# Performance work log

Measured on AMD Instinct MI355X. Metric: run time of the kernel, lower is better.

Reference implementation:

```python
import jax, jax.numpy as jnp
import numpy as np

# NF4 codebook (bitsandbytes nf4 quant_type), 16 levels in [-1, 1]
NF4 = jnp.array([
    -1.0, -0.6961928009986877, -0.5250730514526367, -0.39491748809814453,
    -0.28444138169288635, -0.18477343022823334, -0.09105003625154495, 0.0,
    0.07958029955625534, 0.16093020141124725, 0.24611230194568634,
    0.33791524171829224, 0.44070982933044434, 0.5626170039176941,
    0.7229568362236023, 1.0], dtype=jnp.float32)
BLOCK = 64  # bitsandbytes default quant block size

TOKENS, HD, M = 8192, 4096, 11008


def dequant_nf4(codes, scales):
    # codes: [out, in] int in [0,16); scales: [out, in//BLOCK] per-block absmax
    out_f, in_f = codes.shape
    w = NF4[codes].reshape(out_f, in_f // BLOCK, BLOCK) * scales[:, :, None]
    return w.reshape(out_f, in_f)


def setup_inputs() -> dict:
    key = jax.random.key(0)
    k = jax.random.split(key, 7)
    return {
        "x": jax.random.normal(k[0], (TOKENS, HD), dtype=jnp.float32),
        "gate_codes": jax.random.randint(k[1], (M, HD), 0, 16, dtype=jnp.int32),
        "gate_scales": jax.random.uniform(k[2], (M, HD // BLOCK), dtype=jnp.float32) * 0.1,
        "up_codes": jax.random.randint(k[3], (M, HD), 0, 16, dtype=jnp.int32),
        "up_scales": jax.random.uniform(k[4], (M, HD // BLOCK), dtype=jnp.float32) * 0.1,
        "down_codes": jax.random.randint(k[5], (HD, M), 0, 16, dtype=jnp.int32),
        "down_scales": jax.random.uniform(k[6], (HD, M // BLOCK), dtype=jnp.float32) * 0.1,
    }


def reference(x, gate_codes, gate_scales, up_codes, up_scales, down_codes, down_scales):
    Wg = dequant_nf4(gate_codes, gate_scales)   # [m, hd]
    Wu = dequant_nf4(up_codes, up_scales)       # [m, hd]
    Wd = dequant_nf4(down_codes, down_scales)   # [hd, m]
    g = jnp.einsum('td,md->tm', x, Wg)          # gate_proj(x)
    u = jnp.einsum('td,md->tm', x, Wu)          # up_proj(x)
    h = jax.nn.silu(g) * u                      # SwiGLU
    return jnp.einsum('tm,dm->td', h, Wd)       # down_proj
```

## Files before the change

kernel.cpp:

```cpp
#include <hip/hip_runtime.h>
#include <hip/hip_bf16.h>

typedef _Float16 half8 __attribute__((ext_vector_type(8)));
typedef float floatx4 __attribute__((ext_vector_type(4)));

__device__ __constant__ float NF4_TAB[16] = {
    -1.0f, -0.6961928009986877f, -0.5250730514526367f, -0.39491748809814453f,
    -0.28444138169288635f, -0.18477343022823334f, -0.09105003625154495f, 0.0f,
    0.07958029955625534f, 0.16093020141124725f, 0.24611230194568634f,
    0.33791524171829224f, 0.44070982933044434f, 0.5626170039176941f,
    0.7229568362236023f, 1.0f};

typedef __attribute__((address_space(3))) void lds_t;
typedef __attribute__((address_space(1))) void gbl_t;

__device__ __forceinline__ void gload16(const void* g, void* l) {
  __builtin_amdgcn_global_load_lds((gbl_t*)g, (lds_t*)l, 16, 0, 0);
}

#define FENCE() asm volatile("" ::: "memory")

__global__ void cvt_f32_to_f16_pad(const float* __restrict__ in,
                                   _Float16* __restrict__ out,
                                   int total8, int C8, int OS) {
  int stride = gridDim.x * blockDim.x;
  for (int i = blockIdx.x * blockDim.x + threadIdx.x; i < total8; i += stride) {
    int row = i / C8;
    int col = (i - row * C8) * 8;
    const float4* ip = reinterpret_cast<const float4*>(in + (long)row * (C8 * 8) + col);
    float4 a = ip[0], b = ip[1];
    half8 o;
    o[0] = (_Float16)a.x; o[1] = (_Float16)a.y;
    o[2] = (_Float16)a.z; o[3] = (_Float16)a.w;
    o[4] = (_Float16)b.x; o[5] = (_Float16)b.y;
    o[6] = (_Float16)b.z; o[7] = (_Float16)b.w;
    *reinterpret_cast<half8*>(out + (long)row * OS + col) = o;
  }
}

__global__ void dequant_nf4(const int* __restrict__ codes,
                            const float* __restrict__ scales,
                            _Float16* __restrict__ out,
                            int total8, int C, int CB, int OS) {
  __shared__ float lut[16];
  if (threadIdx.x < 16) lut[threadIdx.x] = NF4_TAB[threadIdx.x];
  __syncthreads();
  int stride = gridDim.x * blockDim.x;
  for (int i = blockIdx.x * blockDim.x + threadIdx.x; i < total8; i += stride) {
    long e = (long)i * 8;
    int row = (int)(e / C);
    int col = (int)(e - (long)row * C);
    float sc = scales[row * CB + (col >> 6)];
    const int4* cp = reinterpret_cast<const int4*>(codes + e);
    int4 c0 = cp[0];
    int4 c1 = cp[1];
    half8 o;
    o[0] = (_Float16)(lut[c0.x & 15] * sc);
    o[1] = (_Float16)(lut[c0.y & 15] * sc);
    o[2] = (_Float16)(lut[c0.z & 15] * sc);
    o[3] = (_Float16)(lut[c0.w & 15] * sc);
    o[4] = (_Float16)(lut[c1.x & 15] * sc);
    o[5] = (_Float16)(lut[c1.y & 15] * sc);
    o[6] = (_Float16)(lut[c1.z & 15] * sc);
    o[7] = (_Float16)(lut[c1.w & 15] * sc);
    *reinterpret_cast<half8*>(out + (long)row * OS + col) = o;
  }
}

template <int K, int LD, int N>
__global__ __launch_bounds__(512, 2) void gemm_fused(
    const _Float16* __restrict__ A,
    const _Float16* __restrict__ G,
    const _Float16* __restrict__ U,
    _Float16* __restrict__ GH) {
  constexpr int NT = K / 64;
  __shared__ __align__(16) _Float16 lds[2 * 32768];

  const int t = threadIdx.x;
  const int lane = t & 63;
  const int wave = t >> 6;
  const int wm = wave >> 2;
  const int wn = wave & 3;

  const int xcd = blockIdx.x & 7;
  const int j = blockIdx.x >> 3;
  const int bm = 4 * xcd + (j & 3);
  const int bn = j >> 2;

  const int lc = (t & 3) ^ ((t >> 3) & 3);
  const _Float16* gA = A + ((long)bm * 256 + (t >> 2)) * LD + lc * 8;
  const _Float16* gG = G + ((long)bn * 128 + (t >> 2)) * LD + lc * 8;
  const _Float16* gU = U + ((long)bn * 128 + (t >> 2)) * LD + lc * 8;
  const long rstep = (long)128 * LD;
  const int dst = t * 8;

  const int rA = wm * 128 + (lane & 15);
  const int rB = wn * 32 + (lane & 15);
  const int ckA = ((lane >> 4) ^ ((rA >> 1) & 3)) * 8;
  const int ckB = ((lane >> 4) ^ ((rB >> 1) & 3)) * 8;
  const int offA = rA * 32 + ckA;
  const int offBG = 16384 + rB * 32 + ckB;
  const int offBU = 24576 + rB * 32 + ckB;

  gload16(gA, lds + dst);
  gload16(gA + rstep, lds + dst + 4096);
  gload16(gG, lds + 16384 + dst);
  gload16(gU, lds + 24576 + dst);
  gload16(gA + 32, lds + 8192 + dst);
  gload16(gA + 32 + rstep, lds + 8192 + dst + 4096);
  gload16(gG + 32, lds + 20480 + dst);
  gload16(gU + 32, lds + 28672 + dst);
  gA += 64; gG += 64; gU += 64;
  asm volatile("s_waitcnt vmcnt(4)" ::: "memory");
  __builtin_amdgcn_s_barrier();
  FENCE();

  floatx4 accG[8][2] = {};
  floatx4 accU[8][2] = {};

  for (int kt = 0; kt < NT; ++kt) {
    const int cb = kt & 1;
    const int sbuf = cb ^ 1;
    const _Float16* lb = lds + cb * 32768;
    _Float16* sb = lds + sbuf * 32768;
    const bool st = (kt + 1 < NT);
    const bool last = (kt == NT - 1);

    half8 a[8], b[2];

#pragma unroll
    for (int i = 0; i < 8; ++i)
      a[i] = *reinterpret_cast<const half8*>(&lb[offA + i * 512]);
    b[0] = *reinterpret_cast<const half8*>(&lb[offBG]);
    b[1] = *reinterpret_cast<const half8*>(&lb[offBG + 512]);
    if (st) { gload16(gA, sb + dst); gload16(gA + rstep, sb + dst + 4096); }
    __builtin_amdgcn_s_barrier();
    FENCE();
    __builtin_amdgcn_s_setprio(1);
#pragma unroll
    for (int i = 0; i < 8; ++i) {
      accG[i][0] = __builtin_amdgcn_mfma_f32_16x16x32_f16(a[i], b[0], accG[i][0], 0, 0, 0);
      accG[i][1] = __builtin_amdgcn_mfma_f32_16x16x32_f16(a[i], b[1], accG[i][1], 0, 0, 0);
    }
    __builtin_amdgcn_s_setprio(0);
    __builtin_amdgcn_s_barrier();
    FENCE();

    b[0] = *reinterpret_cast<const half8*>(&lb[offBU]);
    b[1] = *reinterpret_cast<const half8*>(&lb[offBU + 512]);
    if (st) { gload16(gG, sb + 16384 + dst); gload16(gU, sb + 24576 + dst); }
    if (last) { asm volatile("s_waitcnt vmcnt(0)" ::: "memory"); }
    else      { asm volatile("s_waitcnt vmcnt(4)" ::: "memory"); }
    __builtin_amdgcn_s_barrier();
    FENCE();
    __builtin_amdgcn_s_setprio(1);
#pragma unroll
    for (int i = 0; i < 8; ++i) {
      accU[i][0] = __builtin_amdgcn_mfma_f32_16x16x32_f16(a[i], b[0], accU[i][0], 0, 0, 0);
      accU[i][1] = __builtin_amdgcn_mfma_f32_16x16x32_f16(a[i], b[1], accU[i][1], 0, 0, 0);
    }
    __builtin_amdgcn_s_setprio(0);
    __builtin_amdgcn_s_barrier();
    FENCE();

#pragma unroll
    for (int i = 0; i < 8; ++i)
      a[i] = *reinterpret_cast<const half8*>(&lb[8192 + offA + i * 512]);
    b[0] = *reinterpret_cast<const half8*>(&lb[offBG + 4096]);
    b[1] = *reinterpret_cast<const half8*>(&lb[offBG + 4096 + 512]);
    if (st) { gload16(gA + 32, sb + 8192 + dst); gload16(gA + 32 + rstep, sb + 8192 + dst + 4096); }
    __builtin_amdgcn_s_barrier();
    FENCE();
    __builtin_amdgcn_s_setprio(1);
#pragma unroll
    for (int i = 0; i < 8; ++i) {
      accG[i][0] = __builtin_amdgcn_mfma_f32_16x16x32_f16(a[i], b[0], accG[i][0], 0, 0, 0);
      accG[i][1] = __builtin_amdgcn_mfma_f32_16x16x32_f16(a[i], b[1], accG[i][1], 0, 0, 0);
    }
    __builtin_amdgcn_s_setprio(0);
    __builtin_amdgcn_s_barrier();
    FENCE();

    b[0] = *reinterpret_cast<const half8*>(&lb[offBU + 4096]);
    b[1] = *reinterpret_cast<const half8*>(&lb[offBU + 4096 + 512]);
    if (st) {
      gload16(gG + 32, sb + 20480 + dst);
      gload16(gU + 32, sb + 28672 + dst);
      gA += 64; gG += 64; gU += 64;
    }
    if (!last) { asm volatile("s_waitcnt vmcnt(4)" ::: "memory"); }
    __builtin_amdgcn_s_barrier();
    FENCE();
    __builtin_amdgcn_s_setprio(1);
#pragma unroll
    for (int i = 0; i < 8; ++i) {
      accU[i][0] = __builtin_amdgcn_mfma_f32_16x16x32_f16(a[i], b[0], accU[i][0], 0, 0, 0);
      accU[i][1] = __builtin_amdgcn_mfma_f32_16x16x32_f16(a[i], b[1], accU[i][1], 0, 0, 0);
    }
    __builtin_amdgcn_s_setprio(0);
    __builtin_amdgcn_s_barrier();
    FENCE();
  }

  const int r0 = bm * 256 + wm * 128 + (lane >> 4) * 4;
  const int c0 = bn * 128 + wn * 32 + (lane & 15);
#pragma unroll
  for (int i = 0; i < 8; ++i) {
#pragma unroll
    for (int j2 = 0; j2 < 2; ++j2) {
#pragma unroll
      for (int ii = 0; ii < 4; ++ii) {
        const long idx = (long)(r0 + i * 16 + ii) * N + (c0 + j2 * 16);
        float g = accG[i][j2][ii];
        float u = accU[i][j2][ii];
        GH[idx] = (_Float16)(g / (1.0f + __expf(-g)) * u);
      }
    }
  }
}

template <int K, int LD, int N, int EPI>
__global__ __launch_bounds__(512, 2) void gemm256(
    const _Float16* __restrict__ A,
    const _Float16* __restrict__ B,
    _Float16* __restrict__ GH,
    float* __restrict__ OUT) {
  constexpr int NT = K / 64;
  constexpr int NBC = N / 256;
  __shared__ __align__(16) _Float16 lds[2 * 32768];

  const int t = threadIdx.x;
  const int lane = t & 63;
  const int wave = t >> 6;
  const int wm = wave >> 2;
  const int wn = wave & 3;

  const int xcd = blockIdx.x & 7;
  const int j = blockIdx.x >> 3;
  const int bm = 4 * xcd + (j & 3);
  const int bn = j >> 2;

  const int lc = (t & 3) ^ ((t >> 3) & 3);
  const _Float16* gA = A + ((long)bm * 256 + (t >> 2)) * LD + lc * 8;
  const _Float16* gB = B + ((long)bn * 256 + (t >> 2)) * LD + lc * 8;
  const long rstep = (long)128 * LD;
  const int dst = t * 8;

  const int rA = wm * 128 + (lane & 15);
  const int rB = wn * 64 + (lane & 15);
  const int ckA = ((lane >> 4) ^ ((rA >> 1) & 3)) * 8;
  const int ckB = ((lane >> 4) ^ ((rB >> 1) & 3)) * 8;
  const int offA = rA * 32 + ckA;
  const int offB = 16384 + rB * 32 + ckB;

#define STAGE_SLOT(gp, slab, koff, dbuf)                                   \
  gload16((gp) + (koff), lds + (dbuf) * 32768 + (slab) + dst);             \
  gload16((gp) + (koff) + rstep, lds + (dbuf) * 32768 + (slab) + dst + 4096);

  STAGE_SLOT(gA, 0, 0, 0);
  STAGE_SLOT(gB, 16384, 0, 0);
  STAGE_SLOT(gA, 8192, 32, 0);
  STAGE_SLOT(gB, 24576, 32, 0);
  gA += 64; gB += 64;
  asm volatile("s_waitcnt vmcnt(4)" ::: "memory");
  __builtin_amdgcn_s_barrier();
  FENCE();

  floatx4 acc[8][4] = {};

  for (int kt = 0; kt < NT; ++kt) {
    const int cb = kt & 1;
    const int sbuf = cb ^ 1;
    const _Float16* lb = lds + cb * 32768;
    const bool st = (kt + 1 < NT);
    const bool last = (kt == NT - 1);

    half8 a[8], b[2];

#pragma unroll
    for (int i = 0; i < 8; ++i)
      a[i] = *reinterpret_cast<const half8*>(&lb[offA + i * 512]);
    b[0] = *reinterpret_cast<const half8*>(&lb[offB]);
    b[1] = *reinterpret_cast<const half8*>(&lb[offB + 512]);
    if (st) { STAGE_SLOT(gA, 0, 0, sbuf); }
    __builtin_amdgcn_s_barrier();
    FENCE();
    __builtin_amdgcn_s_setprio(1);
#pragma unroll
    for (int i = 0; i < 8; ++i) {
      acc[i][0] = __builtin_amdgcn_mfma_f32_16x16x32_f16(a[i], b[0], acc[i][0], 0, 0, 0);
      acc[i][1] = __builtin_amdgcn_mfma_f32_16x16x32_f16(a[i], b[1], acc[i][1], 0, 0, 0);
    }
    __builtin_amdgcn_s_setprio(0);
    __builtin_amdgcn_s_barrier();
    FENCE();

    b[0] = *reinterpret_cast<const half8*>(&lb[offB + 2 * 512]);
    b[1] = *reinterpret_cast<const half8*>(&lb[offB + 3 * 512]);
    if (st) { STAGE_SLOT(gB, 16384, 0, sbuf); }
    if (last) { asm volatile("s_waitcnt vmcnt(0)" ::: "memory"); }
    else      { asm volatile("s_waitcnt vmcnt(4)" ::: "memory"); }
    __builtin_amdgcn_s_barrier();
    FENCE();
    __builtin_amdgcn_s_setprio(1);
#pragma unroll
    for (int i = 0; i < 8; ++i) {
      acc[i][2] = __builtin_amdgcn_mfma_f32_16x16x32_f16(a[i], b[0], acc[i][2], 0, 0, 0);
      acc[i][3] = __builtin_amdgcn_mfma_f32_16x16x32_f16(a[i], b[1], acc[i][3], 0, 0, 0);
    }
    __builtin_amdgcn_s_setprio(0);
    __builtin_amdgcn_s_barrier();
    FENCE();

#pragma unroll
    for (int i = 0; i < 8; ++i)
      a[i] = *reinterpret_cast<const half8*>(&lb[8192 + offA + i * 512]);
    b[0] = *reinterpret_cast<const half8*>(&lb[8192 + offB]);
    b[1] = *reinterpret_cast<const half8*>(&lb[8192 + offB + 512]);
    if (st) { STAGE_SLOT(gA, 8192, 32, sbuf); }
    __builtin_amdgcn_s_barrier();
    FENCE();
    __builtin_amdgcn_s_setprio(1);
#pragma unroll
    for (int i = 0; i < 8; ++i) {
      acc[i][0] = __builtin_amdgcn_mfma_f32_16x16x32_f16(a[i], b[0], acc[i][0], 0, 0, 0);
      acc[i][1] = __builtin_amdgcn_mfma_f32_16x16x32_f16(a[i], b[1], acc[i][1], 0, 0, 0);
    }
    __builtin_amdgcn_s_setprio(0);
    __builtin_amdgcn_s_barrier();
    FENCE();

    b[0] = *reinterpret_cast<const half8*>(&lb[8192 + offB + 2 * 512]);
    b[1] = *reinterpret_cast<const half8*>(&lb[8192 + offB + 3 * 512]);
    if (st) { STAGE_SLOT(gB, 24576, 32, sbuf); gA += 64; gB += 64; }
    if (!last) { asm volatile("s_waitcnt vmcnt(4)" ::: "memory"); }
    __builtin_amdgcn_s_barrier();
    FENCE();
    __builtin_amdgcn_s_setprio(1);
#pragma unroll
    for (int i = 0; i < 8; ++i) {
      acc[i][2] = __builtin_amdgcn_mfma_f32_16x16x32_f16(a[i], b[0], acc[i][2], 0, 0, 0);
      acc[i][3] = __builtin_amdgcn_mfma_f32_16x16x32_f16(a[i], b[1], acc[i][3], 0, 0, 0);
    }
    __builtin_amdgcn_s_setprio(0);
    __builtin_amdgcn_s_barrier();
    FENCE();
  }
#undef STAGE_SLOT

  const int r0 = bm * 256 + wm * 128 + (lane >> 4) * 4;
  const int c0 = bn * 256 + wn * 64 + (lane & 15);
#pragma unroll
  for (int i = 0; i < 8; ++i) {
#pragma unroll
    for (int j2 = 0; j2 < 4; ++j2) {
#pragma unroll
      for (int ii = 0; ii < 4; ++ii) {
        const long idx = (long)(r0 + i * 16 + ii) * N + (c0 + j2 * 16);
        if (EPI == 0) {
          GH[idx] = (_Float16)acc[i][j2][ii];
        } else {
          OUT[idx] = acc[i][j2][ii];
        }
      }
    }
  }
}

extern "C" void kernel_launch(void* const* d_in, const int* in_sizes, int n_in,
                              void* d_out, int out_size, void* d_ws, size_t ws_size,
                              hipStream_t stream) {
  const float* x           = (const float*)d_in[0];
  const int*   gate_codes  = (const int*)d_in[1];
  const float* gate_scales = (const float*)d_in[2];
  const int*   up_codes    = (const int*)d_in[3];
  const float* up_scales   = (const float*)d_in[4];
  const int*   down_codes  = (const int*)d_in[5];
  const float* down_scales = (const float*)d_in[6];
  float* out = (float*)d_out;

  const long T = 8192, HD = 4096, M = 11008;

  char* ws = (char*)d_ws;
  _Float16* x16 = (_Float16*)ws;
  _Float16* Wg  = (_Float16*)(ws + T * HD * 2);
  _Float16* Wu  = (_Float16*)(ws + T * HD * 2 + M * HD * 2);
  _Float16* gh  = (_Float16*)(ws + T * HD * 2 + 2 * M * HD * 2);

  cvt_f32_to_f16_pad<<<2048, 256, 0, stream>>>(x, x16, (int)(T * HD / 8),
                                               (int)(HD / 8), (int)HD);
  dequant_nf4<<<2048, 256, 0, stream>>>(gate_codes, gate_scales, Wg,
                                        (int)(M * HD / 8), (int)HD, (int)(HD / 64),
                                        (int)HD);
  dequant_nf4<<<2048, 256, 0, stream>>>(up_codes, up_scales, Wu,
                                        (int)(M * HD / 8), (int)HD, (int)(HD / 64),
                                        (int)HD);

  gemm_fused<4096, 4096, 11008><<<(8192 / 256) * (11008 / 128), 512, 0, stream>>>(
      x16, Wg, Wu, gh);

  dequant_nf4<<<2048, 256, 0, stream>>>(down_codes, down_scales, Wg,
                                        (int)(HD * M / 8), (int)M, (int)(M / 64),
                                        (int)M);
  gemm256<11008, 11008, 4096, 2><<<(8192 / 256) * (4096 / 256), 512, 0, stream>>>(
      gh, Wg, nullptr, out);
}
```

Measured before the change: 2.114 ms.

## Fuse NF4 dequantization of gate/up weights into the fused GEMM B-staging

Replaces the separate dequant kernels for gate and up weights with a pack step that stores 4-bit codes as nibbles in a K-tile-major layout, with transposed scales. The fused GEMM then loads the packed bytes into registers, dequantizes them with byte-permute table lookups and packed fp16 multiplies, and writes the result into swizzled LDS instead of using async global-to-LDS loads for B. This cuts the fp16 weight write-then-read traffic but adds ALU work and LDS stores inside the main loop, plus modified wait counts. Scaling in fp16 (scale cast to half) can change rounding slightly.

```diff
diff --git a/kernel.cpp b/kernel.cpp
--- a/kernel.cpp
+++ b/kernel.cpp
@@ -2,7 +2,9 @@
 #include <hip/hip_bf16.h>
 
 typedef _Float16 half8 __attribute__((ext_vector_type(8)));
+typedef _Float16 h2 __attribute__((ext_vector_type(2)));
 typedef float floatx4 __attribute__((ext_vector_type(4)));
+typedef unsigned int uint;
 
 __device__ __constant__ float NF4_TAB[16] = {
     -1.0f, -0.6961928009986877f, -0.5250730514526367f, -0.39491748809814453f,
@@ -20,28 +22,74 @@
 
 #define FENCE() asm volatile("" ::: "memory")
 
-__global__ void cvt_f32_to_f16_pad(const float* __restrict__ in,
-                                   _Float16* __restrict__ out,
-                                   int total8, int C8, int OS) {
+#if __has_builtin(__builtin_amdgcn_perm)
+#define PERM(a, b, s) __builtin_amdgcn_perm((a), (b), (s))
+#else
+__device__ __forceinline__ uint PERM(uint a, uint b, uint s) {
+  unsigned long long comb = ((unsigned long long)a << 32) | b;
+  uint r = 0;
+#pragma unroll
+  for (int i = 0; i < 4; ++i) {
+    uint idx = (s >> (8 * i)) & 0xFF;
+    uint by = (idx < 8) ? (uint)((comb >> (8 * idx)) & 0xFF) : 0u;
+    r |= by << (8 * i);
+  }
+  return r;
+}
+#endif
+
+#define TL0 0x52339200u
+#define TL1 0x00D4EA8Du
+#define TL2 0x68E02618u
+#define TL3 0x00C9800Du
+#define TH0 0xB6B8B9BCu
+#define TH1 0x00ADB1B4u
+#define TH2 0x3533312Du
+#define TH3 0x3C393837u
+
+__device__ __forceinline__ void deq4(uint s, uint sc2, uint& r0, uint& r1) {
+  uint s7 = s & 0x07070707u;
+  uint m = s & 0x08080808u;
+  uint m8 = (m << 5) - (m >> 3);
+  uint lo = (PERM(TL3, TL2, s7) & m8) | (PERM(TL1, TL0, s) & ~m8);
+  uint hi = (PERM(TH3, TH2, s7) & m8) | (PERM(TH1, TH0, s) & ~m8);
+  uint a0 = PERM(hi, lo, 0x05010400u);
+  uint a1 = PERM(hi, lo, 0x07030602u);
+  h2 v0 = __builtin_bit_cast(h2, a0) * __builtin_bit_cast(h2, sc2);
+  h2 v1 = __builtin_bit_cast(h2, a1) * __builtin_bit_cast(h2, sc2);
+  r0 = __builtin_bit_cast(uint, v0);
+  r1 = __builtin_bit_cast(uint, v1);
+}
+
+__device__ __forceinline__ void deq8(uint d, uint sc2, uint* o) {
+  uint e = d & 0x0F0F0F0Fu;
+  uint od = (d >> 4) & 0x0F0F0F0Fu;
+  uint sA = PERM(od, e, 0x05010400u);
+  uint sB = PERM(od, e, 0x07030602u);
+  deq4(sA, sc2, o[0], o[1]);
+  deq4(sB, sc2, o[2], o[3]);
+}
+
+__global__ void cvt_f32_to_f16(const float* __restrict__ in,
+                               _Float16* __restrict__ out, int total8) {
   int stride = gridDim.x * blockDim.x;
   for (int i = blockIdx.x * blockDim.x + threadIdx.x; i < total8; i += stride) {
-    int row = i / C8;
-    int col = (i - row * C8) * 8;
-    const float4* ip = reinterpret_cast<const float4*>(in + (long)row * (C8 * 8) + col);
+    long e = (long)i * 8;
+    const float4* ip = reinterpret_cast<const float4*>(in + e);
     float4 a = ip[0], b = ip[1];
     half8 o;
     o[0] = (_Float16)a.x; o[1] = (_Float16)a.y;
     o[2] = (_Float16)a.z; o[3] = (_Float16)a.w;
     o[4] = (_Float16)b.x; o[5] = (_Float16)b.y;
     o[6] = (_Float16)b.z; o[7] = (_Float16)b.w;
-    *reinterpret_cast<half8*>(out + (long)row * OS + col) = o;
+    *reinterpret_cast<half8*>(out + e) = o;
   }
 }
 
 __global__ void dequant_nf4(const int* __restrict__ codes,
                             const float* __restrict__ scales,
                             _Float16* __restrict__ out,
-                            int total8, int C, int CB, int OS) {
+                            int total8, int C, int CB) {
   __shared__ float lut[16];
   if (threadIdx.x < 16) lut[threadIdx.x] = NF4_TAB[threadIdx.x];
   __syncthreads();
@@ -63,15 +111,54 @@
     o[5] = (_Float16)(lut[c1.y & 15] * sc);
     o[6] = (_Float16)(lut[c1.z & 15] * sc);
     o[7] = (_Float16)(lut[c1.w & 15] * sc);
-    *reinterpret_cast<half8*>(out + (long)row * OS + col) = o;
+    *reinterpret_cast<half8*>(out + e) = o;
+  }
+}
+
+__global__ void pack_nf4(const int* __restrict__ codes,
+                         unsigned char* __restrict__ pk, int R, int C) {
+  const int CT = C >> 4;
+  const long total = (long)R * CT;
+  const long stride = (long)gridDim.x * blockDim.x;
+  for (long i = blockIdx.x * blockDim.x + threadIdx.x; i < total; i += stride) {
+    int r = (int)(i / CT);
+    int g = (int)(i - (long)r * CT);
+    int c0 = g << 4;
+    const int4* p = reinterpret_cast<const int4*>(codes + (long)r * C + c0);
+    int4 a = p[0], b = p[1], c = p[2], d = p[3];
+    uint w0 = (uint)(a.x & 15) | ((uint)(a.y & 15) << 4) |
+              ((uint)(a.z & 15) << 8) | ((uint)(a.w & 15) << 12) |
+              ((uint)(b.x & 15) << 16) | ((uint)(b.y & 15) << 20) |
+              ((uint)(b.z & 15) << 24) | ((uint)(b.w & 15) << 28);
+    uint w1 = (uint)(c.x & 15) | ((uint)(c.y & 15) << 4) |
+              ((uint)(c.z & 15) << 8) | ((uint)(c.w & 15) << 12) |
+              ((uint)(d.x & 15) << 16) | ((uint)(d.y & 15) << 20) |
+              ((uint)(d.z & 15) << 24) | ((uint)(d.w & 15) << 28);
+    int kt = c0 >> 6;
+    long off = ((long)kt * R + r) * 32 + ((c0 & 63) >> 1);
+    uint2 v; v.x = w0; v.y = w1;
+    *reinterpret_cast<uint2*>(pk + off) = v;
+  }
+}
+
+__global__ void pack_scales(const float* __restrict__ s,
+                            float* __restrict__ o, int R, int CB) {
+  const long total = (long)R * CB;
+  const long stride = (long)gridDim.x * blockDim.x;
+  for (long i = blockIdx.x * blockDim.x + threadIdx.x; i < total; i += stride) {
+    int r = (int)(i / CB);
+    int cb = (int)(i - (long)r * CB);
+    o[(long)cb * R + r] = s[i];
   }
 }
 
 template <int K, int LD, int N>
 __global__ __launch_bounds__(512, 2) void gemm_fused(
     const _Float16* __restrict__ A,
-    const _Float16* __restrict__ G,
-    const _Float16* __restrict__ U,
+    const unsigned char* __restrict__ PKG,
+    const unsigned char* __restrict__ PKU,
+    const float* __restrict__ SCG,
+    const float* __restrict__ SCU,
     _Float16* __restrict__ GH) {
   constexpr int NT = K / 64;
   __shared__ __align__(16) _Float16 lds[2 * 32768];
@@ -89,10 +176,17 @@
 
   const int lc = (t & 3) ^ ((t >> 3) & 3);
   const _Float16* gA = A + ((long)bm * 256 + (t >> 2)) * LD + lc * 8;
-  const _Float16* gG = G + ((long)bn * 128 + (t >> 2)) * LD + lc * 8;
-  const _Float16* gU = U + ((long)bn * 128 + (t >> 2)) * LD + lc * 8;
   const long rstep = (long)128 * LD;
   const int dst = t * 8;
+
+  const int r = t >> 2;
+  const int q = t & 3;
+  const int wh = (r >> 1) & 3;
+  const unsigned char* gPKG = PKG + ((long)(bn * 128 + r)) * 32 + q * 8;
+  const unsigned char* gPKU = PKU + ((long)(bn * 128 + r)) * 32 + q * 8;
+  const float* gSCG = SCG + (bn * 128 + r);
+  const float* gSCU = SCU + (bn * 128 + r);
+  const long pkstep = (long)N * 32;
 
   const int rA = wm * 128 + (lane & 15);
   const int rB = wn * 32 + (lane & 15);
@@ -102,16 +196,54 @@
   const int offBG = 16384 + rB * 32 + ckB;
   const int offBU = 24576 + rB * 32 + ckB;
 
+  uint2 pkg, pku;
+  float scg, scu;
+
+  auto stage_b = [&](int db) {
+    _Float16* base = lds + db * 32768;
+    {
+      _Float16 sh = (_Float16)scg;
+      unsigned short us = __builtin_bit_cast(unsigned short, sh);
+      uint sc2 = (uint)us * 0x10001u;
+      uint o0[4], o1[4];
+      deq8(pkg.x, sc2, o0);
+      deq8(pkg.y, sc2, o1);
+      _Float16* wb = base + 16384 + (q >> 1) * 4096 + r * 32;
+      uint4 v0; v0.x = o0[0]; v0.y = o0[1]; v0.z = o0[2]; v0.w = o0[3];
+      uint4 v1; v1.x = o1[0]; v1.y = o1[1]; v1.z = o1[2]; v1.w = o1[3];
+      *reinterpret_cast<uint4*>(wb + ((2 * (q & 1) + 0) ^ wh) * 8) = v0;
+      *reinterpret_cast<uint4*>(wb + ((2 * (q & 1) + 1) ^ wh) * 8) = v1;
+    }
+    {
+      _Float16 sh = (_Float16)scu;
+      unsigned short us = __builtin_bit_cast(unsigned short, sh);
+      uint sc2 = (uint)us * 0x10001u;
+      uint o0[4], o1[4];
+      deq8(pku.x, sc2, o0);
+      deq8(pku.y, sc2, o1);
+      _Float16* wb = base + 24576 + (q >> 1) * 4096 + r * 32;
+      uint4 v0; v0.x = o0[0]; v0.y = o0[1]; v0.z = o0[2]; v0.w = o0[3];
+      uint4 v1; v1.x = o1[0]; v1.y = o1[1]; v1.z = o1[2]; v1.w = o1[3];
+      *reinterpret_cast<uint4*>(wb + ((2 * (q & 1) + 0) ^ wh) * 8) = v0;
+      *reinterpret_cast<uint4*>(wb + ((2 * (q & 1) + 1) ^ wh) * 8) = v1;
+    }
+  };
+
+  pkg = *reinterpret_cast<const uint2*>(gPKG);
+  pku = *reinterpret_cast<const uint2*>(gPKU);
+  scg = *gSCG;
+  scu = *gSCU;
+  gPKG += pkstep; gPKU += pkstep; gSCG += N; gSCU += N;
+  FENCE();
   gload16(gA, lds + dst);
   gload16(gA + rstep, lds + dst + 4096);
-  gload16(gG, lds + 16384 + dst);
-  gload16(gU, lds + 24576 + dst);
   gload16(gA + 32, lds + 8192 + dst);
   gload16(gA + 32 + rstep, lds + 8192 + dst + 4096);
-  gload16(gG + 32, lds + 20480 + dst);
-  gload16(gU + 32, lds + 28672 + dst);
-  gA += 64; gG += 64; gU += 64;
-  asm volatile("s_waitcnt vmcnt(4)" ::: "memory");
+  gA += 64;
+  FENCE();
+  stage_b(0);
+  asm volatile("s_waitcnt vmcnt(2)" ::: "memory");
+  asm volatile("s_waitcnt lgkmcnt(0)" ::: "memory");
   __builtin_amdgcn_s_barrier();
   FENCE();
 
@@ -133,7 +265,16 @@
       a[i] = *reinterpret_cast<const half8*>(&lb[offA + i * 512]);
     b[0] = *reinterpret_cast<const half8*>(&lb[offBG]);
     b[1] = *reinterpret_cast<const half8*>(&lb[offBG + 512]);
-    if (st) { gload16(gA, sb + dst); gload16(gA + rstep, sb + dst + 4096); }
+    if (st) {
+      pkg = *reinterpret_cast<const uint2*>(gPKG);
+      pku = *reinterpret_cast<const uint2*>(gPKU);
+      scg = *gSCG;
+      scu = *gSCU;
+      gPKG += pkstep; gPKU += pkstep; gSCG += N; gSCU += N;
+      FENCE();
+      gload16(gA, sb + dst);
+      gload16(gA + rstep, sb + dst + 4096);
+    }
     __builtin_amdgcn_s_barrier();
     FENCE();
     __builtin_amdgcn_s_setprio(1);
@@ -148,9 +289,8 @@
 
     b[0] = *reinterpret_cast<const half8*>(&lb[offBU]);
     b[1] = *reinterpret_cast<const half8*>(&lb[offBU + 512]);
-    if (st) { gload16(gG, sb + 16384 + dst); gload16(gU, sb + 24576 + dst); }
     if (last) { asm volatile("s_waitcnt vmcnt(0)" ::: "memory"); }
-    else      { asm volatile("s_waitcnt vmcnt(4)" ::: "memory"); }
+    else      { asm volatile("s_waitcnt vmcnt(6)" ::: "memory"); }
     __builtin_amdgcn_s_barrier();
     FENCE();
     __builtin_amdgcn_s_setprio(1);
@@ -168,7 +308,13 @@
       a[i] = *reinterpret_cast<const half8*>(&lb[8192 + offA + i * 512]);
     b[0] = *reinterpret_cast<const half8*>(&lb[offBG + 4096]);
     b[1] = *reinterpret_cast<const half8*>(&lb[offBG + 4096 + 512]);
-    if (st) { gload16(gA + 32, sb + 8192 + dst); gload16(gA + 32 + rstep, sb + 8192 + dst + 4096); }
+    if (st) {
+      gload16(gA + 32, sb + 8192 + dst);
+      gload16(gA + 32 + rstep, sb + 8192 + dst + 4096);
+      gA += 64;
+      FENCE();
+      stage_b(sbuf);
+    }
     __builtin_amdgcn_s_barrier();
     FENCE();
     __builtin_amdgcn_s_setprio(1);
@@ -178,17 +324,13 @@
       accG[i][1] = __builtin_amdgcn_mfma_f32_16x16x32_f16(a[i], b[1], accG[i][1], 0, 0, 0);
     }
     __builtin_amdgcn_s_setprio(0);
+    asm volatile("s_waitcnt lgkmcnt(0)" ::: "memory");
     __builtin_amdgcn_s_barrier();
     FENCE();
 
     b[0] = *reinterpret_cast<const half8*>(&lb[offBU + 4096]);
     b[1] = *reinterpret_cast<const half8*>(&lb[offBU + 4096 + 512]);
-    if (st) {
-      gload16(gG + 32, sb + 20480 + dst);
-      gload16(gU + 32, sb + 28672 + dst);
-      gA += 64; gG += 64; gU += 64;
-    }
-    if (!last) { asm volatile("s_waitcnt vmcnt(4)" ::: "memory"); }
+    if (st) { asm volatile("s_waitcnt vmcnt(2)" ::: "memory"); }
     __builtin_amdgcn_s_barrier();
     FENCE();
     __builtin_amdgcn_s_setprio(1);
@@ -382,26 +524,25 @@
   const long T = 8192, HD = 4096, M = 11008;
 
   char* ws = (char*)d_ws;
-  _Float16* x16 = (_Float16*)ws;
-  _Float16* Wg  = (_Float16*)(ws + T * HD * 2);
-  _Float16* Wu  = (_Float16*)(ws + T * HD * 2 + M * HD * 2);
-  _Float16* gh  = (_Float16*)(ws + T * HD * 2 + 2 * M * HD * 2);
-
-  cvt_f32_to_f16_pad<<<2048, 256, 0, stream>>>(x, x16, (int)(T * HD / 8),
-                                               (int)(HD / 8), (int)HD);
-  dequant_nf4<<<2048, 256, 0, stream>>>(gate_codes, gate_scales, Wg,
-                                        (int)(M * HD / 8), (int)HD, (int)(HD / 64),
-                                        (int)HD);
-  dequant_nf4<<<2048, 256, 0, stream>>>(up_codes, up_scales, Wu,
-                                        (int)(M * HD / 8), (int)HD, (int)(HD / 64),
-                                        (int)HD);
+  _Float16* x16 = (_Float16*)ws;                   ws += T * HD * 2;
+  unsigned char* pkG = (unsigned char*)ws;         ws += M * HD / 2;
+  unsigned char* pkU = (unsigned char*)ws;         ws += M * HD / 2;
+  float* scG = (float*)ws;                         ws += (HD / 64) * M * 4;
+  float* scU = (float*)ws;                         ws += (HD / 64) * M * 4;
+  _Float16* Wd = (_Float16*)ws;                    ws += HD * M * 2;
+  _Float16* gh = (_Float16*)ws;
+
+  cvt_f32_to_f16<<<2048, 256, 0, stream>>>(x, x16, (int)(T * HD / 8));
+  pack_nf4<<<2048, 256, 0, stream>>>(gate_codes, pkG, (int)M, (int)HD);
+  pack_nf4<<<2048, 256, 0, stream>>>(up_codes, pkU, (int)M, (int)HD);
+  pack_scales<<<2048, 256, 0, stream>>>(gate_scales, scG, (int)M, (int)(HD / 64));
+  pack_scales<<<2048, 256, 0, stream>>>(up_scales, scU, (int)M, (int)(HD / 64));
 
   gemm_fused<4096, 4096, 11008><<<(8192 / 256) * (11008 / 128), 512, 0, stream>>>(
-      x16, Wg, Wu, gh);
-
-  dequant_nf4<<<2048, 256, 0, stream>>>(down_codes, down_scales, Wg,
-                                        (int)(HD * M / 8), (int)M, (int)(M / 64),
-                                        (int)M);
+      x16, pkG, pkU, scG, scU, gh);
+
+  dequant_nf4<<<2048, 256, 0, stream>>>(down_codes, down_scales, Wd,
+                                        (int)(HD * M / 8), (int)M, (int)(M / 64));
   gemm256<11008, 11008, 4096, 2><<<(8192 / 256) * (4096 / 256), 512, 0, stream>>>(
-      gh, Wg, nullptr, out);
-}
+      gh, Wd, nullptr, out);
+}
```

Result: slower. 2.324 ms (+9.9%).
